# Performance work log

Measured on AMD Instinct MI355X. Metric: run time of the kernel, lower is better.

## Reference

```python
import jax, jax.numpy as jnp
import numpy as np

N = 50000
E = 800000
C_IN, C_HID, C_OUT = 512, 128, 2
HEADS2 = 3
NEG_SLOPE = 0.2


def gat_conv(x, src, dst, W, att_src, att_dst, bias, heads, ch, concat):
    """PyG GATConv (eval mode) on pre-augmented (self-loop included) edge lists.
    x: [N, F_in], W: [F_in, heads*ch], att_*: [heads, ch], bias: [heads*ch] or [ch].
    """
    n = x.shape[0]
    h = (x @ W).reshape(n, heads, ch)                 # [N, H, C]
    a_src = (h * att_src).sum(-1)                     # [N, H]
    a_dst = (h * att_dst).sum(-1)                     # [N, H]
    e = jax.nn.leaky_relu(a_src[src] + a_dst[dst], NEG_SLOPE)  # [E', H]
    # segment softmax over edges sharing a destination node
    m = jax.ops.segment_max(e, dst, num_segments=n)
    m = jnp.where(jnp.isfinite(m), m, 0.0)
    ex = jnp.exp(e - m[dst])
    denom = jax.ops.segment_sum(ex, dst, num_segments=n)
    alpha = ex / (denom[dst] + 1e-16)                 # [E', H]
    out = jax.ops.segment_sum(h[src] * alpha[:, :, None], dst, num_segments=n)  # [N, H, C]
    out = out.reshape(n, heads * ch) if concat else out.mean(axis=1)
    return out + bias


def setup_inputs() -> dict:
    key = jax.random.key(0)
    ks = jax.random.split(key, 12)
    x = jax.random.normal(ks[0], (N, C_IN), dtype=jnp.float32)
    edge_index = jax.random.randint(ks[1], (2, E), 0, N, dtype=jnp.int64)
    s1 = 1.0 / np.sqrt(C_IN)
    s2 = 1.0 / np.sqrt(C_HID)
    return {
        "x": x,
        "edge_index": edge_index,
        "W1": jax.random.normal(ks[2], (C_IN, C_HID), dtype=jnp.float32) * s1,
        "att_src1": jax.random.normal(ks[3], (1, C_HID), dtype=jnp.float32) * s2,
        "att_dst1": jax.random.normal(ks[4], (1, C_HID), dtype=jnp.float32) * s2,
        "bias1": jnp.zeros((C_HID,), dtype=jnp.float32),
        "W2": jax.random.normal(ks[5], (C_HID, HEADS2 * C_OUT), dtype=jnp.float32) * s2,
        "att_src2": jax.random.normal(ks[6], (HEADS2, C_OUT), dtype=jnp.float32) * 0.5,
        "att_dst2": jax.random.normal(ks[7], (HEADS2, C_OUT), dtype=jnp.float32) * 0.5,
        "bias2": jnp.zeros((C_OUT,), dtype=jnp.float32),
    }


def reference(x, edge_index, W1, att_src1, att_dst1, bias1, W2, att_src2, att_dst2, bias2):
    n = x.shape[0]
    loop = jnp.arange(n, dtype=edge_index.dtype)
    src = jnp.concatenate([edge_index[0], loop])      # PyG add_self_loops=True
    dst = jnp.concatenate([edge_index[1], loop])
    h = gat_conv(x, src, dst, W1, att_src1, att_dst1, bias1, 1, C_HID, True)
    h = jax.nn.relu(h)                                # Dropout is identity in eval
    out = gat_conv(h, src, dst, W2, att_src2, att_dst2, bias2, HEADS2, C_OUT, False)
    return out
```

## Files before the change

### kernel.cpp

```cpp
#include <hip/hip_runtime.h>

#define N_NODES 50000
#define N_EDGES 800000
#define E_TOT   850000
#define C_IN    512
#define C_HID   128
#define NEG     0.2f

typedef _Float16 f16x8 __attribute__((ext_vector_type(8)));
typedef __attribute__((ext_vector_type(4))) float f32x4;

__device__ __forceinline__ float leaky(float x) { return x > 0.f ? x : NEG * x; }

union U32H2 { unsigned u; _Float16 h[2]; float f; };
union BFrag { uint4 u; f16x8 h; };

__device__ __forceinline__ unsigned short f2h(float f) {
  U32H2 c; c.h[0] = (_Float16)f; return (unsigned short)(c.u & 0xffff);
}

__device__ __forceinline__ unsigned pk2h(float a, float b) {
  union { __fp16 v __attribute__((ext_vector_type(2))); unsigned u; } c;
  c.v = __builtin_amdgcn_cvt_pkrtz(a, b);
  return c.u;
}

__global__ __launch_bounds__(256) void setup_kernel(
    const float* __restrict__ W1, const float* __restrict__ as1,
    const float* __restrict__ ad1, const int* __restrict__ ei,
    unsigned short* __restrict__ Wswz, float* __restrict__ v1s, float* __restrict__ v1d,
    int* __restrict__ deg, int* __restrict__ rnk) {
  const int b = blockIdx.x;
  if (b < 32) {
    int t = b * 256 + threadIdx.x;
    int c = t >> 6, kc = t & 63;
    if (c >= C_HID) return;
    int kblk = kc >> 2, q = kc & 3;
    int ct = c >> 4, l15 = c & 15;
    int lane = q * 16 + l15;
    unsigned short hb[8], lb[8];
#pragma unroll
    for (int i = 0; i < 8; i++) {
      float w = W1[(size_t)(kc * 8 + i) * C_HID + c];
      _Float16 hi = (_Float16)w;
      _Float16 lo = (_Float16)(w - (float)hi);
      U32H2 ch; ch.h[0] = hi;
      U32H2 cl; cl.h[0] = lo;
      hb[i] = (unsigned short)(ch.u & 0xffff);
      lb[i] = (unsigned short)(cl.u & 0xffff);
    }
    size_t chunk0 = ((size_t)(kblk * 8 + ct) * 2) * 512;
    *(uint4*)&Wswz[chunk0 + (size_t)lane * 8]       = *(uint4*)hb;
    *(uint4*)&Wswz[chunk0 + 512 + (size_t)lane * 8] = *(uint4*)lb;
  } else if (b < 160) {
    const int wv = threadIdx.x >> 6, lane = threadIdx.x & 63;
    const int k = (b - 32) * 4 + wv;
    if (k >= C_IN) return;
    float2 w = *(const float2*)(W1 + (size_t)k * C_HID + 2 * lane);
    float2 a = *(const float2*)(as1 + 2 * lane);
    float2 d = *(const float2*)(ad1 + 2 * lane);
    float s = w.x * a.x + w.y * a.y;
    float t = w.x * d.x + w.y * d.y;
#pragma unroll
    for (int m = 32; m >= 1; m >>= 1) {
      s += __shfl_xor(s, m, 64);
      t += __shfl_xor(t, m, 64);
    }
    if (lane == 0) { v1s[k] = s; v1d[k] = t; }
  } else {
    int e = (b - 160) * 256 + threadIdx.x;
    if (e < N_EDGES) rnk[e] = atomicAdd(&deg[ei[N_EDGES + e]], 1);
  }
}

__global__ __launch_bounds__(256) void lin1_kernel(const float* __restrict__ x,
    const unsigned short* __restrict__ Wswz,
    const float* __restrict__ v1s, const float* __restrict__ v1d,
    unsigned short* __restrict__ h1u, float* __restrict__ a_src, float* __restrict__ a_dst) {
  __shared__ __attribute__((aligned(16))) unsigned short As[2][64][40];

  const int tid  = threadIdx.x;
  const int lane = tid & 63, wv = tid >> 6;
  const int m0   = blockIdx.x * 64;

  const int arow = tid >> 2, kseg = (tid & 3) * 8;
  int grow = m0 + arow;
  if (grow >= N_NODES) grow = N_NODES - 1;
  const float* xrow = x + (size_t)grow * C_IN + kseg;

  f32x4 acc[4][2];
#pragma unroll
  for (int rt = 0; rt < 4; rt++) { acc[rt][0] = (f32x4)0.f; acc[rt][1] = (f32x4)0.f; }
  float ps = 0.f, pd = 0.f;

  const int q = lane >> 4, l15 = lane & 15;

  float4 xa = *(const float4*)(xrow);
  float4 xb = *(const float4*)(xrow + 4);

#pragma unroll
  for (int kblk = 0; kblk < 16; kblk++) {
    const int k0 = kblk * 32;
    const int buf = kblk & 1;
    float4 vsa = *(const float4*)(v1s + k0 + kseg);
    float4 vsb = *(const float4*)(v1s + k0 + kseg + 4);
    float4 vda = *(const float4*)(v1d + k0 + kseg);
    float4 vdb = *(const float4*)(v1d + k0 + kseg + 4);
    ps += xa.x * vsa.x + xa.y * vsa.y + xa.z * vsa.z + xa.w * vsa.w
        + xb.x * vsb.x + xb.y * vsb.y + xb.z * vsb.z + xb.w * vsb.w;
    pd += xa.x * vda.x + xa.y * vda.y + xa.z * vda.z + xa.w * vda.w
        + xb.x * vdb.x + xb.y * vdb.y + xb.z * vdb.z + xb.w * vdb.w;
    *(uint4*)&As[buf][arow][kseg] = make_uint4(pk2h(xa.x, xa.y), pk2h(xa.z, xa.w),
                                               pk2h(xb.x, xb.y), pk2h(xb.z, xb.w));
    __syncthreads();
    if (kblk < 15) {
      xa = *(const float4*)(xrow + k0 + 32);
      xb = *(const float4*)(xrow + k0 + 36);
    }

    const unsigned short* bp = Wswz + ((size_t)(kblk * 8 + wv * 2) * 2) * 512 + (size_t)lane * 8;
    BFrag b00, b01, b10, b11;
    b00.u = *(const uint4*)(bp);
    b01.u = *(const uint4*)(bp + 512);
    b10.u = *(const uint4*)(bp + 1024);
    b11.u = *(const uint4*)(bp + 1536);

#pragma unroll
    for (int rt = 0; rt < 4; rt++) {
      f16x8 af = *(const f16x8*)&As[buf][rt * 16 + l15][q * 8];
      acc[rt][0] = __builtin_amdgcn_mfma_f32_16x16x32_f16(af, b00.h, acc[rt][0], 0, 0, 0);
      acc[rt][0] = __builtin_amdgcn_mfma_f32_16x16x32_f16(af, b01.h, acc[rt][0], 0, 0, 0);
      acc[rt][1] = __builtin_amdgcn_mfma_f32_16x16x32_f16(af, b10.h, acc[rt][1], 0, 0, 0);
      acc[rt][1] = __builtin_amdgcn_mfma_f32_16x16x32_f16(af, b11.h, acc[rt][1], 0, 0, 0);
    }
  }

  ps += __shfl_xor(ps, 1, 64); ps += __shfl_xor(ps, 2, 64);
  pd += __shfl_xor(pd, 1, 64); pd += __shfl_xor(pd, 2, 64);
  if ((tid & 3) == 0) {
    int row = m0 + arow;
    if (row < N_NODES) { a_src[row] = ps; a_dst[row] = pd; }
  }

#pragma unroll
  for (int rt = 0; rt < 4; rt++) {
    int rbase = m0 + rt * 16 + q * 4;
#pragma unroll
    for (int ct = 0; ct < 2; ct++) {
      int col = wv * 32 + ct * 16 + l15;
#pragma unroll
      for (int ri = 0; ri < 4; ri++) {
        int row = rbase + ri;
        if (row < N_NODES)
          h1u[(size_t)row * C_HID + col] = f2h(acc[rt][ct][ri]);
      }
    }
  }
}

__global__ __launch_bounds__(1024) void scan_kernel(const int* __restrict__ deg,
                                                    int* __restrict__ rowptr) {
  __shared__ int wsum[16];
  const int tid = threadIdx.x, lane = tid & 63, wv = tid >> 6;
  int carry = 0;
  for (int base = 0; base < N_NODES; base += 8192) {
    int i0 = base + tid * 8;
    int v[8];
    if (i0 + 8 <= N_NODES) {
      int4 va = *(const int4*)(deg + i0);
      int4 vb = *(const int4*)(deg + i0 + 4);
      v[0]=va.x+1; v[1]=va.y+1; v[2]=va.z+1; v[3]=va.w+1;
      v[4]=vb.x+1; v[5]=vb.y+1; v[6]=vb.z+1; v[7]=vb.w+1;
    } else {
#pragma unroll
      for (int i = 0; i < 8; i++) v[i] = (i0 + i < N_NODES) ? deg[i0 + i] + 1 : 0;
    }
    int tsum = 0;
#pragma unroll
    for (int i = 0; i < 8; i++) tsum += v[i];
    int sc = tsum;
#pragma unroll
    for (int off = 1; off < 64; off <<= 1) {
      int t = __shfl_up(sc, off, 64);
      if (lane >= off) sc += t;
    }
    if (lane == 63) wsum[wv] = sc;
    __syncthreads();
    if (wv == 0 && lane < 16) {
      int s = wsum[lane];
#pragma unroll
      for (int off = 1; off < 16; off <<= 1) {
        int t = __shfl_up(s, off, 64);
        if (lane >= off) s += t;
      }
      wsum[lane] = s;
    }
    __syncthreads();
    int ex = carry + (wv ? wsum[wv - 1] : 0) + sc - tsum;
#pragma unroll
    for (int i = 0; i < 8; i++) {
      if (i0 + i < N_NODES) rowptr[i0 + i] = ex;
      ex += v[i];
    }
    carry += wsum[15];
    __syncthreads();
  }
  if (tid == 0) rowptr[N_NODES] = carry;
}

__global__ void bucket_kernel(const int* __restrict__ ei, const int* __restrict__ rnk,
                              const int* __restrict__ rowptr,
                              const float* __restrict__ a_src, const float* __restrict__ a_dst,
                              int2* __restrict__ esw) {
  int e = blockIdx.x * blockDim.x + threadIdx.x;
  if (e >= E_TOT) return;
  int src, slot;
  if (e < N_EDGES) {
    src = ei[e];
    int dst = ei[N_EDGES + e];
    slot = rowptr[dst] + rnk[e];
    U32H2 c; c.f = __expf(leaky(a_src[src] + a_dst[dst]));
    esw[slot] = make_int2(src, (int)c.u);
  } else {
    int n = e - N_EDGES;
    slot = rowptr[n + 1] - 1;
    U32H2 c; c.f = __expf(leaky(a_src[n] + a_dst[n]));
    esw[slot] = make_int2(n, (int)c.u);
  }
}

__global__ __launch_bounds__(256) void agg1_kernel(const unsigned short* __restrict__ h1u,
    const int2* __restrict__ esw, const int* __restrict__ rowptr,
    const float* __restrict__ bias1, const float* __restrict__ W2,
    const float* __restrict__ as2w, const float* __restrict__ ad2w,
    float* __restrict__ hs2) {
  const int wv = threadIdx.x >> 6, lane = threadIdx.x & 63;
  const int q = lane >> 4, r = lane & 15;
  const int n = blockIdx.x * 4 + wv;
  const int start = rowptr[n], end = rowptr[n + 1];

  float w2reg[8][6];
#pragma unroll
  for (int j = 0; j < 8; j++) {
    const float* w2r = W2 + (size_t)(r * 8 + j) * 6;
#pragma unroll
    for (int o = 0; o < 6; o++) w2reg[j][o] = w2r[o];
  }
  float4 ba = *(const float4*)(bias1 + r * 8);
  float4 bb = *(const float4*)(bias1 + r * 8 + 4);

  const unsigned short* hbase = h1u + r * 8;

  float acc[8] = {0, 0, 0, 0, 0, 0, 0, 0};
  float wsum = 0.f;
  for (int base = start; base < end; base += 64) {
    int idx = base + lane;
    int sreg = 0; float wreg = 0.f;
    if (idx < end) {
      int2 sv = esw[idx];
      sreg = sv.x;
      U32H2 c; c.u = (unsigned)sv.y;
      wreg = c.f;
    }
    wsum += wreg;
    const int cnt = min(64, end - base);
#pragma unroll
    for (int i = 0; i < 4; i++) {
      if (i * 16 >= cnt) break;
      int   s0 = __shfl(sreg, i * 16 + q, 64);
      int   s1 = __shfl(sreg, i * 16 + 4 + q, 64);
      int   s2 = __shfl(sreg, i * 16 + 8 + q, 64);
      int   s3 = __shfl(sreg, i * 16 + 12 + q, 64);
      float w0 = __shfl(wreg, i * 16 + q, 64);
      float w1 = __shfl(wreg, i * 16 + 4 + q, 64);
      float w2 = __shfl(wreg, i * 16 + 8 + q, 64);
      float w3 = __shfl(wreg, i * 16 + 12 + q, 64);
      uint4 g0 = *(const uint4*)(hbase + (size_t)s0 * C_HID);
      uint4 g1 = *(const uint4*)(hbase + (size_t)s1 * C_HID);
      uint4 g2 = *(const uint4*)(hbase + (size_t)s2 * C_HID);
      uint4 g3 = *(const uint4*)(hbase + (size_t)s3 * C_HID);
      U32H2 c0, c1, c2, c3;
#define ACC8(G, W) \
      c0.u = G.x; c1.u = G.y; c2.u = G.z; c3.u = G.w; \
      acc[0] = fmaf(W, (float)c0.h[0], acc[0]); acc[1] = fmaf(W, (float)c0.h[1], acc[1]); \
      acc[2] = fmaf(W, (float)c1.h[0], acc[2]); acc[3] = fmaf(W, (float)c1.h[1], acc[3]); \
      acc[4] = fmaf(W, (float)c2.h[0], acc[4]); acc[5] = fmaf(W, (float)c2.h[1], acc[5]); \
      acc[6] = fmaf(W, (float)c3.h[0], acc[6]); acc[7] = fmaf(W, (float)c3.h[1], acc[7]);
      ACC8(g0, w0) ACC8(g1, w1) ACC8(g2, w2) ACC8(g3, w3)
#undef ACC8
    }
  }

#pragma unroll
  for (int i = 0; i < 8; i++) {
    acc[i] += __shfl_xor(acc[i], 16, 64);
    acc[i] += __shfl_xor(acc[i], 32, 64);
  }
#pragma unroll
  for (int m = 32; m >= 1; m >>= 1) wsum += __shfl_xor(wsum, m, 64);
  const float inv = 1.f / wsum;

  float u[8] = {fmaxf(acc[0] * inv + ba.x, 0.f), fmaxf(acc[1] * inv + ba.y, 0.f),
                fmaxf(acc[2] * inv + ba.z, 0.f), fmaxf(acc[3] * inv + ba.w, 0.f),
                fmaxf(acc[4] * inv + bb.x, 0.f), fmaxf(acc[5] * inv + bb.y, 0.f),
                fmaxf(acc[6] * inv + bb.z, 0.f), fmaxf(acc[7] * inv + bb.w, 0.f)};
  float p[6] = {0, 0, 0, 0, 0, 0};
#pragma unroll
  for (int j = 0; j < 8; j++)
#pragma unroll
    for (int o = 0; o < 6; o++) p[o] = fmaf(u[j], w2reg[j][o], p[o]);
#pragma unroll
  for (int o = 0; o < 6; o++) {
    p[o] += __shfl_xor(p[o], 1, 64);
    p[o] += __shfl_xor(p[o], 2, 64);
    p[o] += __shfl_xor(p[o], 4, 64);
    p[o] += __shfl_xor(p[o], 8, 64);
  }

  if (lane == 0) {
    float as0 = p[0] * as2w[0] + p[1] * as2w[1];
    float as1 = p[2] * as2w[2] + p[3] * as2w[3];
    float as2_ = p[4] * as2w[4] + p[5] * as2w[5];
    float ad0 = p[0] * ad2w[0] + p[1] * ad2w[1];
    float ad1 = p[2] * ad2w[2] + p[3] * ad2w[3];
    float ad2_ = p[4] * ad2w[4] + p[5] * ad2w[5];
    float* dst = hs2 + (size_t)n * 12;
    *(float4*)(dst)     = make_float4(p[0], p[1], p[2], p[3]);
    *(float4*)(dst + 4) = make_float4(p[4], p[5], as0, as1);
    *(float4*)(dst + 8) = make_float4(as2_, ad0, ad1, ad2_);
  }
}

__global__ __launch_bounds__(256) void agg2_kernel(const float* __restrict__ hs2,
    const int* __restrict__ rowptr, const int2* __restrict__ esw,
    const float* __restrict__ bias2, float* __restrict__ out) {
  const int wv = threadIdx.x >> 6, lane = threadIdx.x & 63;
  const int q = lane >> 4, r = lane & 15;
  const int n = blockIdx.x * 16 + wv * 4 + q;
  if (n >= N_NODES) return;
  const int start = rowptr[n], end = rowptr[n + 1];
  float4 own = *(const float4*)(hs2 + (size_t)n * 12 + 8);
  const float ad0 = own.y, ad1 = own.z, ad2 = own.w;

  float d0 = 0.f, d1 = 0.f, d2 = 0.f;
  float a0 = 0.f, a1 = 0.f, a2 = 0.f, a3 = 0.f, a4 = 0.f, a5 = 0.f;
  for (int j = start + r; j < end; j += 16) {
    int s = esw[j].x;
    const float* rec = hs2 + (size_t)s * 12;
    float4 A = *(const float4*)(rec);
    float4 B = *(const float4*)(rec + 4);
    float  C = rec[8];
    float e0 = __expf(leaky(B.z + ad0));
    float e1 = __expf(leaky(B.w + ad1));
    float e2 = __expf(leaky(C + ad2));
    d0 += e0; d1 += e1; d2 += e2;
    a0 += e0 * A.x; a1 += e0 * A.y;
    a2 += e1 * A.z; a3 += e1 * A.w;
    a4 += e2 * B.x; a5 += e2 * B.y;
  }
#pragma unroll
  for (int m = 8; m >= 1; m >>= 1) {
    d0 += __shfl_xor(d0, m, 64); d1 += __shfl_xor(d1, m, 64); d2 += __shfl_xor(d2, m, 64);
    a0 += __shfl_xor(a0, m, 64); a1 += __shfl_xor(a1, m, 64); a2 += __shfl_xor(a2, m, 64);
    a3 += __shfl_xor(a3, m, 64); a4 += __shfl_xor(a4, m, 64); a5 += __shfl_xor(a5, m, 64);
  }
  if (r == 0) {
    float o0 = (a0 / d0 + a2 / d1 + a4 / d2) * (1.f / 3.f) + bias2[0];
    float o1 = (a1 / d0 + a3 / d1 + a5 / d2) * (1.f / 3.f) + bias2[1];
    *(float2*)(out + (size_t)n * 2) = make_float2(o0, o1);
  }
}

extern "C" void kernel_launch(void* const* d_in, const int* in_sizes, int n_in,
                              void* d_out, int out_size, void* d_ws, size_t ws_size,
                              hipStream_t stream) {
  const float* x        = (const float*)d_in[0];
  const int*   ei       = (const int*)d_in[1];
  const float* W1       = (const float*)d_in[2];
  const float* att_src1 = (const float*)d_in[3];
  const float* att_dst1 = (const float*)d_in[4];
  const float* bias1    = (const float*)d_in[5];
  const float* W2       = (const float*)d_in[6];
  const float* att_src2 = (const float*)d_in[7];
  const float* att_dst2 = (const float*)d_in[8];
  const float* bias2    = (const float*)d_in[9];
  float* out = (float*)d_out;

  char* w = (char*)d_ws;
  auto alloc = [&](size_t bytes) {
    char* p = w;
    w += (bytes + 255) & ~(size_t)255;
    return p;
  };
  unsigned short* h1u    = (unsigned short*)alloc((size_t)N_NODES * C_HID * 2);
  unsigned short* Wswz   = (unsigned short*)alloc((size_t)C_IN * C_HID * 2 * 2);
  float*          v1s    = (float*)alloc((size_t)C_IN * 4);
  float*          v1d    = (float*)alloc((size_t)C_IN * 4);
  float*          a_src1 = (float*)alloc((size_t)N_NODES * 4);
  float*          a_dst1 = (float*)alloc((size_t)N_NODES * 4);
  int*            deg    = (int*)alloc((size_t)N_NODES * 4);
  int*            rowptr = (int*)alloc((size_t)(N_NODES + 4) * 4);
  int*            rnk    = (int*)alloc((size_t)N_EDGES * 4);
  int2*           esw    = (int2*)alloc((size_t)E_TOT * 8);
  float*          hs2    = (float*)alloc((size_t)N_NODES * 12 * 4);

  (void)hipMemsetAsync(deg, 0, (size_t)N_NODES * 4, stream);

  setup_kernel<<<160 + (N_EDGES + 255) / 256, 256, 0, stream>>>(
      W1, att_src1, att_dst1, ei, Wswz, v1s, v1d, deg, rnk);
  scan_kernel<<<1, 1024, 0, stream>>>(deg, rowptr);
  lin1_kernel<<<(N_NODES + 63) / 64, 256, 0, stream>>>(x, Wswz, v1s, v1d,
                                                       h1u, a_src1, a_dst1);
  bucket_kernel<<<(E_TOT + 255) / 256, 256, 0, stream>>>(ei, rnk, rowptr,
                                                         a_src1, a_dst1, esw);
  agg1_kernel<<<N_NODES / 4, 256, 0, stream>>>(h1u, esw, rowptr, bias1, W2,
                                               att_src2, att_dst2, hs2);
  agg2_kernel<<<(N_NODES + 15) / 16, 256, 0, stream>>>(hs2, rowptr, esw, bias2, out);
}
```

Baseline: 331.8 us.

## Fold degree scan into lin1 extra block and batch agg1 gathers by eight

Removes the separate single-block scan kernel and runs the degree prefix scan in one extra 256-thread block appended to the lin1 GEMM grid, so the scan overlaps with the GEMM and one launch is saved. The scan block handles 2048 elements per iteration instead of 8192, so it takes more serial iterations. In agg1, neighbor gathers are issued eight at a time before the FMAs, giving more memory-level parallelism per wave. Loading W2 and bias is moved after the edge loop to reduce register pressure during that loop. The wider batches still raise register use per wave, which could lower occupancy.

```diff
diff --git a/kernel.cpp b/kernel.cpp
--- a/kernel.cpp
+++ b/kernel.cpp
@@ -76,8 +76,59 @@
 __global__ __launch_bounds__(256) void lin1_kernel(const float* __restrict__ x,
     const unsigned short* __restrict__ Wswz,
     const float* __restrict__ v1s, const float* __restrict__ v1d,
-    unsigned short* __restrict__ h1u, float* __restrict__ a_src, float* __restrict__ a_dst) {
+    unsigned short* __restrict__ h1u, float* __restrict__ a_src, float* __restrict__ a_dst,
+    const int* __restrict__ deg, int* __restrict__ rowptr) {
   __shared__ __attribute__((aligned(16))) unsigned short As[2][64][40];
+  __shared__ int wsum[4];
+
+  if (blockIdx.x == gridDim.x - 1) {
+    const int tid = threadIdx.x, lane = tid & 63, wv = tid >> 6;
+    int carry = 0;
+    for (int base = 0; base < N_NODES; base += 2048) {
+      int i0 = base + tid * 8;
+      int v[8];
+      if (i0 + 8 <= N_NODES) {
+        int4 va = *(const int4*)(deg + i0);
+        int4 vb = *(const int4*)(deg + i0 + 4);
+        v[0]=va.x+1; v[1]=va.y+1; v[2]=va.z+1; v[3]=va.w+1;
+        v[4]=vb.x+1; v[5]=vb.y+1; v[6]=vb.z+1; v[7]=vb.w+1;
+      } else {
+#pragma unroll
+        for (int i = 0; i < 8; i++) v[i] = (i0 + i < N_NODES) ? deg[i0 + i] + 1 : 0;
+      }
+      int tsum = 0;
+#pragma unroll
+      for (int i = 0; i < 8; i++) tsum += v[i];
+      int sc = tsum;
+#pragma unroll
+      for (int off = 1; off < 64; off <<= 1) {
+        int t = __shfl_up(sc, off, 64);
+        if (lane >= off) sc += t;
+      }
+      if (lane == 63) wsum[wv] = sc;
+      __syncthreads();
+      if (tid < 4) {
+        int s = wsum[tid];
+#pragma unroll
+        for (int off = 1; off < 4; off <<= 1) {
+          int t = __shfl_up(s, off, 64);
+          if (tid >= off) s += t;
+        }
+        wsum[tid] = s;
+      }
+      __syncthreads();
+      int ex = carry + (wv ? wsum[wv - 1] : 0) + sc - tsum;
+#pragma unroll
+      for (int i = 0; i < 8; i++) {
+        if (i0 + i < N_NODES) rowptr[i0 + i] = ex;
+        ex += v[i];
+      }
+      carry += wsum[3];
+      __syncthreads();
+    }
+    if (tid == 0) rowptr[N_NODES] = carry;
+    return;
+  }
 
   const int tid  = threadIdx.x;
   const int lane = tid & 63, wv = tid >> 6;
@@ -156,56 +207,6 @@
       }
     }
   }
-}
-
-__global__ __launch_bounds__(1024) void scan_kernel(const int* __restrict__ deg,
-                                                    int* __restrict__ rowptr) {
-  __shared__ int wsum[16];
-  const int tid = threadIdx.x, lane = tid & 63, wv = tid >> 6;
-  int carry = 0;
-  for (int base = 0; base < N_NODES; base += 8192) {
-    int i0 = base + tid * 8;
-    int v[8];
-    if (i0 + 8 <= N_NODES) {
-      int4 va = *(const int4*)(deg + i0);
-      int4 vb = *(const int4*)(deg + i0 + 4);
-      v[0]=va.x+1; v[1]=va.y+1; v[2]=va.z+1; v[3]=va.w+1;
-      v[4]=vb.x+1; v[5]=vb.y+1; v[6]=vb.z+1; v[7]=vb.w+1;
-    } else {
-#pragma unroll
-      for (int i = 0; i < 8; i++) v[i] = (i0 + i < N_NODES) ? deg[i0 + i] + 1 : 0;
-    }
-    int tsum = 0;
-#pragma unroll
-    for (int i = 0; i < 8; i++) tsum += v[i];
-    int sc = tsum;
-#pragma unroll
-    for (int off = 1; off < 64; off <<= 1) {
-      int t = __shfl_up(sc, off, 64);
-      if (lane >= off) sc += t;
-    }
-    if (lane == 63) wsum[wv] = sc;
-    __syncthreads();
-    if (wv == 0 && lane < 16) {
-      int s = wsum[lane];
-#pragma unroll
-      for (int off = 1; off < 16; off <<= 1) {
-        int t = __shfl_up(s, off, 64);
-        if (lane >= off) s += t;
-      }
-      wsum[lane] = s;
-    }
-    __syncthreads();
-    int ex = carry + (wv ? wsum[wv - 1] : 0) + sc - tsum;
-#pragma unroll
-    for (int i = 0; i < 8; i++) {
-      if (i0 + i < N_NODES) rowptr[i0 + i] = ex;
-      ex += v[i];
-    }
-    carry += wsum[15];
-    __syncthreads();
-  }
-  if (tid == 0) rowptr[N_NODES] = carry;
 }
 
 __global__ void bucket_kernel(const int* __restrict__ ei, const int* __restrict__ rnk,
@@ -239,16 +240,6 @@
   const int n = blockIdx.x * 4 + wv;
   const int start = rowptr[n], end = rowptr[n + 1];
 
-  float w2reg[8][6];
-#pragma unroll
-  for (int j = 0; j < 8; j++) {
-    const float* w2r = W2 + (size_t)(r * 8 + j) * 6;
-#pragma unroll
-    for (int o = 0; o < 6; o++) w2reg[j][o] = w2r[o];
-  }
-  float4 ba = *(const float4*)(bias1 + r * 8);
-  float4 bb = *(const float4*)(bias1 + r * 8 + 4);
-
   const unsigned short* hbase = h1u + r * 8;
 
   float acc[8] = {0, 0, 0, 0, 0, 0, 0, 0};
@@ -264,31 +255,32 @@
     }
     wsum += wreg;
     const int cnt = min(64, end - base);
-#pragma unroll
-    for (int i = 0; i < 4; i++) {
-      if (i * 16 >= cnt) break;
-      int   s0 = __shfl(sreg, i * 16 + q, 64);
-      int   s1 = __shfl(sreg, i * 16 + 4 + q, 64);
-      int   s2 = __shfl(sreg, i * 16 + 8 + q, 64);
-      int   s3 = __shfl(sreg, i * 16 + 12 + q, 64);
-      float w0 = __shfl(wreg, i * 16 + q, 64);
-      float w1 = __shfl(wreg, i * 16 + 4 + q, 64);
-      float w2 = __shfl(wreg, i * 16 + 8 + q, 64);
-      float w3 = __shfl(wreg, i * 16 + 12 + q, 64);
-      uint4 g0 = *(const uint4*)(hbase + (size_t)s0 * C_HID);
-      uint4 g1 = *(const uint4*)(hbase + (size_t)s1 * C_HID);
-      uint4 g2 = *(const uint4*)(hbase + (size_t)s2 * C_HID);
-      uint4 g3 = *(const uint4*)(hbase + (size_t)s3 * C_HID);
-      U32H2 c0, c1, c2, c3;
-#define ACC8(G, W) \
-      c0.u = G.x; c1.u = G.y; c2.u = G.z; c3.u = G.w; \
-      acc[0] = fmaf(W, (float)c0.h[0], acc[0]); acc[1] = fmaf(W, (float)c0.h[1], acc[1]); \
-      acc[2] = fmaf(W, (float)c1.h[0], acc[2]); acc[3] = fmaf(W, (float)c1.h[1], acc[3]); \
-      acc[4] = fmaf(W, (float)c2.h[0], acc[4]); acc[5] = fmaf(W, (float)c2.h[1], acc[5]); \
-      acc[6] = fmaf(W, (float)c3.h[0], acc[6]); acc[7] = fmaf(W, (float)c3.h[1], acc[7]);
-      ACC8(g0, w0) ACC8(g1, w1) ACC8(g2, w2) ACC8(g3, w3)
-#undef ACC8
-    }
+
+    auto batch = [&](int B) {
+      int s[8]; float w[8];
+#pragma unroll
+      for (int j = 0; j < 8; j++) {
+        int pos = B + j * 4 + q;
+        s[j] = __shfl(sreg, pos, 64);
+        w[j] = __shfl(wreg, pos, 64);
+      }
+      uint4 g[8];
+#pragma unroll
+      for (int j = 0; j < 8; j++)
+        g[j] = *(const uint4*)(hbase + (size_t)s[j] * C_HID);
+#pragma unroll
+      for (int j = 0; j < 8; j++) {
+        U32H2 c0, c1, c2, c3;
+        c0.u = g[j].x; c1.u = g[j].y; c2.u = g[j].z; c3.u = g[j].w;
+        const float W = w[j];
+        acc[0] = fmaf(W, (float)c0.h[0], acc[0]); acc[1] = fmaf(W, (float)c0.h[1], acc[1]);
+        acc[2] = fmaf(W, (float)c1.h[0], acc[2]); acc[3] = fmaf(W, (float)c1.h[1], acc[3]);
+        acc[4] = fmaf(W, (float)c2.h[0], acc[4]); acc[5] = fmaf(W, (float)c2.h[1], acc[5]);
+        acc[6] = fmaf(W, (float)c3.h[0], acc[6]); acc[7] = fmaf(W, (float)c3.h[1], acc[7]);
+      }
+    };
+    batch(0);
+    if (cnt > 32) batch(32);
   }
 
 #pragma unroll
@@ -299,6 +291,16 @@
 #pragma unroll
   for (int m = 32; m >= 1; m >>= 1) wsum += __shfl_xor(wsum, m, 64);
   const float inv = 1.f / wsum;
+
+  float w2reg[8][6];
+#pragma unroll
+  for (int j = 0; j < 8; j++) {
+    const float* w2r = W2 + (size_t)(r * 8 + j) * 6;
+#pragma unroll
+    for (int o = 0; o < 6; o++) w2reg[j][o] = w2r[o];
+  }
+  float4 ba = *(const float4*)(bias1 + r * 8);
+  float4 bb = *(const float4*)(bias1 + r * 8 + 4);
 
   float u[8] = {fmaxf(acc[0] * inv + ba.x, 0.f), fmaxf(acc[1] * inv + ba.y, 0.f),
                 fmaxf(acc[2] * inv + ba.z, 0.f), fmaxf(acc[3] * inv + ba.w, 0.f),
@@ -408,9 +410,9 @@
 
   setup_kernel<<<160 + (N_EDGES + 255) / 256, 256, 0, stream>>>(
       W1, att_src1, att_dst1, ei, Wswz, v1s, v1d, deg, rnk);
-  scan_kernel<<<1, 1024, 0, stream>>>(deg, rowptr);
-  lin1_kernel<<<(N_NODES + 63) / 64, 256, 0, stream>>>(x, Wswz, v1s, v1d,
-                                                       h1u, a_src1, a_dst1);
+  lin1_kernel<<<(N_NODES + 63) / 64 + 1, 256, 0, stream>>>(x, Wswz, v1s, v1d,
+                                                           h1u, a_src1, a_dst1,
+                                                           deg, rowptr);
   bucket_kernel<<<(E_TOT + 255) / 256, 256, 0, stream>>>(ei, rnk, rowptr,
                                                          a_src1, a_dst1, esw);
   agg1_kernel<<<N_NODES / 4, 256, 0, stream>>>(h1u, esw, rowptr, bias1, W2,
```

Result: no change. 336.7 us (+1.5%).
